# Performance work log

Hardware: AMD Instinct MI355X
Metric: run time of the kernel (lower is better)

## Reference

```python
import jax, jax.numpy as jnp
import numpy as np

B = 1024        # number of language embeddings in the batch
D = 128         # language embedding dim
N_LANGS = 8000  # number of ISO language codes in the metric caches


def setup_inputs() -> dict:
    key = jax.random.key(0)
    k1, k2, k3 = jax.random.split(key, 3)
    language_ids = jax.random.randint(k1, (B,), 0, N_LANGS, dtype=jnp.int64)
    language_embeddings = jax.random.normal(k2, (B, D), dtype=jnp.float32)
    # Precomputed metric distance table: (tree_dist/max + map_dist/max + (1-asp_sim)) / 3
    # In the original this is a dict-of-dicts lookup; here it is a dense [L, L] gather table.
    metric_dist = jax.random.uniform(k3, (N_LANGS, N_LANGS), dtype=jnp.float32)
    return {
        "language_ids": language_ids,
        "language_embeddings": language_embeddings,
        "metric_dist": metric_dist,
    }


def reference(language_ids, language_embeddings, metric_dist):
    # Pairwise mean-L1 distance between all embeddings: [B, B]
    # (L1Loss with default 'mean' reduction => mean over the D axis)
    embed_dist = jnp.mean(
        jnp.abs(language_embeddings[:, None, :] - language_embeddings[None, :, :]),
        axis=-1,
    )
    # Gather precomputed metric distances for every (lang_i, lang_j) pair: [B, B]
    md = metric_dist[language_ids[:, None], language_ids[None, :]]
    # Original loop skips pairs with equal language ids (includes both orders otherwise)
    mask = (language_ids[:, None] != language_ids[None, :]).astype(embed_dist.dtype)
    per_pair = jnp.abs(embed_dist - md) * mask
    # sum(losses) / len(losses) over the included pairs
    return per_pair.sum() / mask.sum()
```

## Files before the change

kernel.cpp:

```cpp
#include <hip/hip_runtime.h>

#define NB    1024
#define ND    128
#define NLANG 8000

#define TILE    32
#define NPAIR   16
#define PSTRIDE 65
#define NBLK  ((NB / TILE) * (NB / TILE))

__global__ __launch_bounds__(256) void lesl_main(
    const int*   __restrict__ ids,
    const float* __restrict__ emb,
    const float* __restrict__ md,
    float*       __restrict__ partials)
{
    __shared__ float4 sI[NPAIR * PSTRIDE];
    __shared__ float4 sJ[NPAIR * PSTRIDE];
    __shared__ float  red[8];

    const int tid = threadIdx.x;
    const int bi  = blockIdx.x & 31;
    const int bj  = blockIdx.x >> 5;
    const int i0  = bi * TILE;
    const int j0  = bj * TILE;

    const int tx = tid & 15;
    const int ty = tid >> 4;

    const int i_a  = i0 + (ty << 1);
    const int j_a  = j0 + (tx << 1);
    const int idi0 = ids[i_a];
    const int idi1 = ids[i_a + 1];
    const int idj0 = ids[j_a];
    const int idj1 = ids[j_a + 1];
    const float m00 = md[(size_t)idi0 * NLANG + idj0];
    const float m01 = md[(size_t)idi0 * NLANG + idj1];
    const float m10 = md[(size_t)idi1 * NLANG + idj0];
    const float m11 = md[(size_t)idi1 * NLANG + idj1];

    const float4* embv = (const float4*)emb;
    for (int k = tid; k < TILE * (ND / 4); k += 256) {
        const int r   = k >> 5;
        const int c   = k & 31;
        const int dst = (r >> 1) * PSTRIDE + (c << 1) + (r & 1);
        sI[dst] = embv[(size_t)(i0 + r) * (ND / 4) + c];
        sJ[dst] = embv[(size_t)(j0 + r) * (ND / 4) + c];
    }
    __syncthreads();

    const float4* pI = &sI[ty * PSTRIDE];
    const float4* pJ = &sJ[tx * PSTRIDE];

    float4 a00 = {0,0,0,0}, a01 = {0,0,0,0}, a10 = {0,0,0,0}, a11 = {0,0,0,0};

#define ACC(A, X, Y)                              \
    A.x += __builtin_fabsf(X.x - Y.x);            \
    A.y += __builtin_fabsf(X.y - Y.y);            \
    A.z += __builtin_fabsf(X.z - Y.z);            \
    A.w += __builtin_fabsf(X.w - Y.w);

    #pragma unroll 4
    for (int c = 0; c < 32; ++c) {
        const float4 x0 = pI[2 * c];
        const float4 x1 = pI[2 * c + 1];
        const float4 y0 = pJ[2 * c];
        const float4 y1 = pJ[2 * c + 1];
        ACC(a00, x0, y0);
        ACC(a01, x0, y1);
        ACC(a10, x1, y0);
        ACC(a11, x1, y1);
    }
#undef ACC

    float s = 0.0f, cnt = 0.0f;
    auto contrib = [&](const float4& A, int ia, int ib, float m) {
        const float sad  = (A.x + A.y) + (A.z + A.w);
        const float diff = __builtin_fabsf(sad * 0.0078125f - m);
        if (ia != ib) { s += diff; cnt += 1.0f; }
    };
    contrib(a00, idi0, idj0, m00);
    contrib(a01, idi0, idj1, m01);
    contrib(a10, idi1, idj0, m10);
    contrib(a11, idi1, idj1, m11);

    #pragma unroll
    for (int off = 32; off > 0; off >>= 1) {
        s   += __shfl_down(s,   off, 64);
        cnt += __shfl_down(cnt, off, 64);
    }
    const int wid = tid >> 6;
    if ((tid & 63) == 0) { red[wid] = s; red[4 + wid] = cnt; }
    __syncthreads();
    if (tid == 0) {
        float S = red[0] + red[1] + red[2] + red[3];
        float C = red[4] + red[5] + red[6] + red[7];
        ((float2*)partials)[blockIdx.x] = make_float2(S, C);
    }
}

__global__ __launch_bounds__(256) void lesl_reduce(
    const float* __restrict__ partials, float* __restrict__ out)
{
    __shared__ float red[8];
    const int tid = threadIdx.x;
    const float2* p = (const float2*)partials;

    float s = 0.0f, c = 0.0f;
    #pragma unroll
    for (int k = 0; k < 4; ++k) {
        const float2 v = p[tid * 4 + k];
        s += v.x; c += v.y;
    }
    #pragma unroll
    for (int off = 32; off > 0; off >>= 1) {
        s += __shfl_down(s, off, 64);
        c += __shfl_down(c, off, 64);
    }
    const int wid = tid >> 6;
    if ((tid & 63) == 0) { red[wid] = s; red[4 + wid] = c; }
    __syncthreads();
    if (tid == 0) {
        const float S = red[0] + red[1] + red[2] + red[3];
        const float C = red[4] + red[5] + red[6] + red[7];
        out[0] = S / C;
    }
}

extern "C" void kernel_launch(void* const* d_in, const int* in_sizes, int n_in,
                              void* d_out, int out_size, void* d_ws, size_t ws_size,
                              hipStream_t stream) {
    const int*   ids = (const int*)d_in[0];
    const float* emb = (const float*)d_in[1];
    const float* md  = (const float*)d_in[2];
    float* out = (float*)d_out;
    float* ws  = (float*)d_ws;

    lesl_main<<<dim3(NBLK), dim3(256), 0, stream>>>(ids, emb, md, ws);
    lesl_reduce<<<dim3(1), dim3(256), 0, stream>>>(ws, out);
}
```

Baseline: 307.4 us.

## Enlarge tiles to 64x64 with 4x4 register micro-tile per thread

Raises the block tile from 32x32 to 64x64 pairs and has each thread compute a 4x4 block of embedding pairs instead of 2x2, with a matching shared-memory layout and a reduce kernel that reads 256 partials. This lifts register-level reuse of loaded embedding vectors, cutting LDS traffic per arithmetic op and global re-loading of the embeddings. In exchange it uses 64 accumulator registers per thread plus gathered metric values, and the grid shrinks to 256 blocks, which may lower occupancy or leave some of the GPU's compute units idle.

```diff
diff --git a/kernel.cpp b/kernel.cpp
--- a/kernel.cpp
+++ b/kernel.cpp
@@ -2,12 +2,20 @@
 
 #define NB    1024
 #define ND    128
+#define NF4   32
 #define NLANG 8000
 
-#define TILE    32
-#define NPAIR   16
-#define PSTRIDE 65
-#define NBLK  ((NB / TILE) * (NB / TILE))
+#define TILE    64
+#define NGRP    16
+#define GSTRIDE 129
+#define NBLK    256
+
+__device__ __forceinline__ void acc4(float4& A, const float4 X, const float4 Y) {
+    A.x += __builtin_fabsf(X.x - Y.x);
+    A.y += __builtin_fabsf(X.y - Y.y);
+    A.z += __builtin_fabsf(X.z - Y.z);
+    A.w += __builtin_fabsf(X.w - Y.w);
+}
 
 __global__ __launch_bounds__(256) void lesl_main(
     const int*   __restrict__ ids,
@@ -15,74 +23,84 @@
     const float* __restrict__ md,
     float*       __restrict__ partials)
 {
-    __shared__ float4 sI[NPAIR * PSTRIDE];
-    __shared__ float4 sJ[NPAIR * PSTRIDE];
+    __shared__ float4 sI[NGRP * GSTRIDE];
+    __shared__ float4 sJ[NGRP * GSTRIDE];
     __shared__ float  red[8];
 
     const int tid = threadIdx.x;
-    const int bi  = blockIdx.x & 31;
-    const int bj  = blockIdx.x >> 5;
+    const int bi  = blockIdx.x & 15;
+    const int bj  = blockIdx.x >> 4;
     const int i0  = bi * TILE;
     const int j0  = bj * TILE;
 
     const int tx = tid & 15;
     const int ty = tid >> 4;
 
-    const int i_a  = i0 + (ty << 1);
-    const int j_a  = j0 + (tx << 1);
-    const int idi0 = ids[i_a];
-    const int idi1 = ids[i_a + 1];
-    const int idj0 = ids[j_a];
-    const int idj1 = ids[j_a + 1];
-    const float m00 = md[(size_t)idi0 * NLANG + idj0];
-    const float m01 = md[(size_t)idi0 * NLANG + idj1];
-    const float m10 = md[(size_t)idi1 * NLANG + idj0];
-    const float m11 = md[(size_t)idi1 * NLANG + idj1];
+    int iid[4], jid[4];
+    #pragma unroll
+    for (int w = 0; w < 4; ++w) {
+        iid[w] = ids[i0 + (ty << 2) + w];
+        jid[w] = ids[j0 + (tx << 2) + w];
+    }
+    float mdv[4][4];
+    #pragma unroll
+    for (int a = 0; a < 4; ++a) {
+        #pragma unroll
+        for (int b = 0; b < 4; ++b) {
+            mdv[a][b] = md[(size_t)iid[a] * NLANG + jid[b]];
+        }
+    }
 
     const float4* embv = (const float4*)emb;
-    for (int k = tid; k < TILE * (ND / 4); k += 256) {
+    for (int k = tid; k < TILE * NF4; k += 256) {
         const int r   = k >> 5;
         const int c   = k & 31;
-        const int dst = (r >> 1) * PSTRIDE + (c << 1) + (r & 1);
-        sI[dst] = embv[(size_t)(i0 + r) * (ND / 4) + c];
-        sJ[dst] = embv[(size_t)(j0 + r) * (ND / 4) + c];
+        const int dst = (r >> 2) * GSTRIDE + ((r & 3) << 5) + c;
+        sI[dst] = embv[(size_t)(i0 + r) * NF4 + c];
+        sJ[dst] = embv[(size_t)(j0 + r) * NF4 + c];
     }
     __syncthreads();
 
-    const float4* pI = &sI[ty * PSTRIDE];
-    const float4* pJ = &sJ[tx * PSTRIDE];
+    const float4* pI = &sI[ty * GSTRIDE];
+    const float4* pJ = &sJ[tx * GSTRIDE];
 
-    float4 a00 = {0,0,0,0}, a01 = {0,0,0,0}, a10 = {0,0,0,0}, a11 = {0,0,0,0};
-
-#define ACC(A, X, Y)                              \
-    A.x += __builtin_fabsf(X.x - Y.x);            \
-    A.y += __builtin_fabsf(X.y - Y.y);            \
-    A.z += __builtin_fabsf(X.z - Y.z);            \
-    A.w += __builtin_fabsf(X.w - Y.w);
+    float4 acc[4][4];
+    #pragma unroll
+    for (int a = 0; a < 4; ++a) {
+        #pragma unroll
+        for (int b = 0; b < 4; ++b) {
+            acc[a][b] = make_float4(0.f, 0.f, 0.f, 0.f);
+        }
+    }
 
     #pragma unroll 4
     for (int c = 0; c < 32; ++c) {
-        const float4 x0 = pI[2 * c];
-        const float4 x1 = pI[2 * c + 1];
-        const float4 y0 = pJ[2 * c];
-        const float4 y1 = pJ[2 * c + 1];
-        ACC(a00, x0, y0);
-        ACC(a01, x0, y1);
-        ACC(a10, x1, y0);
-        ACC(a11, x1, y1);
+        float4 x[4], y[4];
+        #pragma unroll
+        for (int w = 0; w < 4; ++w) {
+            x[w] = pI[(w << 5) + c];
+            y[w] = pJ[(w << 5) + c];
+        }
+        #pragma unroll
+        for (int a = 0; a < 4; ++a) {
+            #pragma unroll
+            for (int b = 0; b < 4; ++b) {
+                acc4(acc[a][b], x[a], y[b]);
+            }
+        }
     }
-#undef ACC
 
     float s = 0.0f, cnt = 0.0f;
-    auto contrib = [&](const float4& A, int ia, int ib, float m) {
-        const float sad  = (A.x + A.y) + (A.z + A.w);
-        const float diff = __builtin_fabsf(sad * 0.0078125f - m);
-        if (ia != ib) { s += diff; cnt += 1.0f; }
-    };
-    contrib(a00, idi0, idj0, m00);
-    contrib(a01, idi0, idj1, m01);
-    contrib(a10, idi1, idj0, m10);
-    contrib(a11, idi1, idj1, m11);
+    #pragma unroll
+    for (int a = 0; a < 4; ++a) {
+        #pragma unroll
+        for (int b = 0; b < 4; ++b) {
+            const float4 A = acc[a][b];
+            const float sad  = (A.x + A.y) + (A.z + A.w);
+            const float diff = __builtin_fabsf(sad * 0.0078125f - mdv[a][b]);
+            if (iid[a] != jid[b]) { s += diff; cnt += 1.0f; }
+        }
+    }
 
     #pragma unroll
     for (int off = 32; off > 0; off >>= 1) {
@@ -93,8 +111,8 @@
     if ((tid & 63) == 0) { red[wid] = s; red[4 + wid] = cnt; }
     __syncthreads();
     if (tid == 0) {
-        float S = red[0] + red[1] + red[2] + red[3];
-        float C = red[4] + red[5] + red[6] + red[7];
+        const float S = red[0] + red[1] + red[2] + red[3];
+        const float C = red[4] + red[5] + red[6] + red[7];
         ((float2*)partials)[blockIdx.x] = make_float2(S, C);
     }
 }
@@ -104,14 +122,9 @@
 {
     __shared__ float red[8];
     const int tid = threadIdx.x;
-    const float2* p = (const float2*)partials;
+    const float2 v = ((const float2*)partials)[tid];
 
-    float s = 0.0f, c = 0.0f;
-    #pragma unroll
-    for (int k = 0; k < 4; ++k) {
-        const float2 v = p[tid * 4 + k];
-        s += v.x; c += v.y;
-    }
+    float s = v.x, c = v.y;
     #pragma unroll
     for (int off = 32; off > 0; off >>= 1) {
         s += __shfl_down(s, off, 64);
```

Result: no change. 313.5 us (+2.0%).
